# Kernel tuning notes

Measured on AMD Instinct MI355X. Metric: run time of the kernel, lower is better.

The kernel has to match this reference:

```python
import jax, jax.numpy as jnp
import numpy as np

# TT decomposition config (from Eff_TTEmbedding args in source)
P = (216, 216, 216)      # auto-factorized p_shapes for n=10,000,000 (216^3 >= n)
Q = (2, 4, 2)            # tt_q_shapes, prod = 16 = embedding_dim
R = (128, 128)           # tt_ranks
NUM_TABLES = 2
BATCH = 1024
NUM_EMB = 10_000_000


def setup_inputs() -> dict:
    key = jax.random.key(0)
    k0, k1, k2, k3 = jax.random.split(key, 4)
    # sparse indices per TT table: [n_tables, batch]
    lS_i = jax.random.randint(k3, (NUM_TABLES, BATCH), 0, NUM_EMB, dtype=jnp.int64)
    # TT cores, weight_dist='uniform'
    core0 = jax.random.uniform(k0, (NUM_TABLES, P[0], Q[0] * R[0]), dtype=jnp.float32, minval=-0.01, maxval=0.01)
    core1 = jax.random.uniform(k1, (NUM_TABLES, P[1], R[0] * Q[1] * R[1]), dtype=jnp.float32, minval=-0.01, maxval=0.01)
    core2 = jax.random.uniform(k2, (NUM_TABLES, P[2], R[1] * Q[2]), dtype=jnp.float32, minval=-0.01, maxval=0.01)
    return {"lS_i": lS_i, "core0": core0, "core1": core1, "core2": core2}


def _tt_lookup(idx, c0, c1, c2):
    """TT embedding lookup for one table. idx: [B] int; returns [B, prod(Q)]."""
    B = idx.shape[0]
    # mixed-radix decomposition of flat index into (i0, i1, i2)
    i0 = idx // (P[1] * P[2])
    i1 = (idx // P[2]) % P[1]
    i2 = idx % P[2]
    # gather TT core slices (the memory-bound irregular access)
    A = c0[i0].reshape(B, Q[0], R[0])            # [B, 2, 128]
    Bm = c1[i1].reshape(B, R[0], Q[1] * R[1])    # [B, 128, 512]
    C = c2[i2].reshape(B, R[1], Q[2])            # [B, 128, 2]
    # chained small matmuls along TT ranks
    AB = jnp.einsum('bqr,brs->bqs', A, Bm).reshape(B, Q[0] * Q[1], R[1])  # [B, 8, 128]
    out = jnp.einsum('bqr,brs->bqs', AB, C)      # [B, 8, 2]
    return out.reshape(B, Q[0] * Q[1] * Q[2])    # [B, 16]


def reference(lS_i, core0, core1, core2):
    # per-table dispatch (forward returns one embedding bag per TT table)
    return jax.vmap(_tt_lookup)(lS_i, core0, core1, core2)  # [n_tables, B, 16]
```

## Files before the change

kernel.cpp:

```cpp
#include <hip/hip_runtime.h>


#define NGROUPS 432
#define NLOOK   2048

__global__ __launch_bounds__(512) void tt_prep(const int* __restrict__ idx32,
                                               int* __restrict__ w) {
    __shared__ int cnt[NGROUPS];
    __shared__ int wtot[8];
    __shared__ int cursor[NGROUPS];
    const int tid  = threadIdx.x;
    const int lane = tid & 63;
    const int wv   = tid >> 6;

    for (int i = tid; i < NGROUPS; i += 512) cnt[i] = 0;
    __syncthreads();

    const bool is64 = (idx32[1] == 0) & (idx32[3] == 0) &
                      (idx32[5] == 0) & (idx32[7] == 0);

    int grp[4];
#pragma unroll
    for (int j = 0; j < 4; ++j) {
        const int id = tid + j * 512;
        const unsigned idx = is64 ? (unsigned)((const long long*)idx32)[id]
                                  : (unsigned)idx32[id];
        const unsigned i0  = idx / 46656u;
        const unsigned rem = idx - i0 * 46656u;
        const unsigned i1  = rem / 216u;
        const unsigned i2  = rem - i1 * 216u;
        const int table = id >> 10;
        grp[j] = table * 216 + (int)i1;
        w[2912 + id] = (int)((i0 << 16) | i2);
        atomicAdd(&cnt[grp[j]], 1);
    }
    __syncthreads();

    const int v = (tid < NGROUPS) ? cnt[tid] : 0;
    int s = v;
#pragma unroll
    for (int d = 1; d < 64; d <<= 1) {
        const int t = __shfl_up(s, d);
        if (lane >= d) s += t;
    }
    if (lane == 63) wtot[wv] = s;
    __syncthreads();
    int off = 0;
    for (int i = 0; i < wv; ++i) off += wtot[i];
    if (tid < NGROUPS) {
        const int st = s + off - v;
        w[tid]       = st;
        w[432 + tid] = v;
        cursor[tid]  = st;
    }
    __syncthreads();

#pragma unroll
    for (int j = 0; j < 4; ++j) {
        const int id  = tid + j * 512;
        const int pos = atomicAdd(&cursor[grp[j]], 1);
        w[864 + pos] = id;
    }
}

__global__ __launch_bounds__(128) void tt_main(
    const float* __restrict__ c0,
    const float* __restrict__ c1,
    const float* __restrict__ c2,
    const int* __restrict__ w,
    float* __restrict__ out)
{
    const int g  = blockIdx.x;
    const int q  = blockIdx.y;
    const int cs = blockIdx.z;
    const int m = w[432 + g];
    if (m <= cs * 8) return;
    const int s0    = w[g];
    const int table = g / 216;
    const int i1    = g - table * 216;

    const int tid = threadIdx.x;
    const int rh  = tid >> 6;
    const int tl  = tid & 63;

    __shared__ float lds[2048];
    float2* lds2 = (float2*)lds;
    __shared__ int s_id[8];
    __shared__ int s_aux[8];

    const float2* b2 = (const float2*)(c1 + (((size_t)(table * 216 + i1)) << 16))
                       + (size_t)rh * 64 * 256 + (q * 64 + tl);
    const float* c0t = c0 + (size_t)table * 216 * 256;

    for (int base = cs * 8; base < m; base += 16) {
        const int cl = min(8, m - base);
        __syncthreads();
        if (tid < 8) {
            const bool ok = tid < cl;
            const int id  = ok ? w[864 + s0 + base + tid] : 0;
            s_id[tid]  = id;
            s_aux[tid] = ok ? w[2912 + id] : 0;
        }
        __syncthreads();

#pragma unroll
        for (int l = 0; l < 8; ++l) {
            const float* ar = c0t + (size_t)(s_aux[l] >> 16) * 256;
#pragma unroll
            for (int k = 0; k < 2; ++k) {
                const int e = tid + 128 * k;
                lds[l * 256 + 2 * (e & 127) + (e >> 7)] = ar[e];
            }
        }
        __syncthreads();

        float2 acc[8][2];
#pragma unroll
        for (int l = 0; l < 8; ++l) {
            acc[l][0] = make_float2(0.f, 0.f);
            acc[l][1] = make_float2(0.f, 0.f);
        }

#pragma unroll 8
        for (int rr = 0; rr < 64; ++rr) {
            const float2 bv = b2[(size_t)rr * 256];
            const int r = rh * 64 + rr;
#pragma unroll
            for (int l = 0; l < 8; ++l) {
                const float2 av = lds2[l * 128 + r];
                acc[l][0].x += av.x * bv.x; acc[l][0].y += av.x * bv.y;
                acc[l][1].x += av.y * bv.x; acc[l][1].y += av.y * bv.y;
            }
        }

        __syncthreads();
        if (rh == 1) {
#pragma unroll
            for (int l = 0; l < 8; ++l) {
                lds2[(l * 2 + 0) * 64 + tl] = acc[l][0];
                lds2[(l * 2 + 1) * 64 + tl] = acc[l][1];
            }
        }
        __syncthreads();

        if (rh == 0) {
#pragma unroll
            for (int l = 0; l < 8; ++l) {
                const float2 t0 = lds2[(l * 2 + 0) * 64 + tl];
                const float2 t1 = lds2[(l * 2 + 1) * 64 + tl];
                const float a0x = acc[l][0].x + t0.x, a0y = acc[l][0].y + t0.y;
                const float a1x = acc[l][1].x + t1.x, a1y = acc[l][1].y + t1.y;
                if (l < cl) {
                    const float* crow = c2 + (size_t)(table * 216 + (s_aux[l] & 0xffff)) * 256;
                    const float4 cv = *(const float4*)(crow + 4 * tl);
                    float p00 = a0x * cv.x + a0y * cv.z;
                    float p01 = a0x * cv.y + a0y * cv.w;
                    float p10 = a1x * cv.x + a1y * cv.z;
                    float p11 = a1x * cv.y + a1y * cv.w;
#pragma unroll
                    for (int mm = 32; mm >= 1; mm >>= 1) {
                        p00 += __shfl_xor(p00, mm);
                        p01 += __shfl_xor(p01, mm);
                        p10 += __shfl_xor(p10, mm);
                        p11 += __shfl_xor(p11, mm);
                    }
                    if (tl == 0) {
                        float* o = out + (size_t)s_id[l] * 16;
                        o[q * 2 + 0]     = p00;
                        o[q * 2 + 1]     = p01;
                        o[8 + q * 2 + 0] = p10;
                        o[8 + q * 2 + 1] = p11;
                    }
                }
            }
        }
    }
}

extern "C" void kernel_launch(void* const* d_in, const int* in_sizes, int n_in,
                              void* d_out, int out_size, void* d_ws, size_t ws_size,
                              hipStream_t stream) {
    const int*   idx = (const int*)d_in[0];
    const float* c0  = (const float*)d_in[1];
    const float* c1  = (const float*)d_in[2];
    const float* c2  = (const float*)d_in[3];
    float* out = (float*)d_out;
    int* w = (int*)d_ws;

    tt_prep<<<dim3(1), dim3(512), 0, stream>>>(idx, w);
    tt_main<<<dim3(NGROUPS, 4, 2), dim3(128), 0, stream>>>(c0, c1, c2, w, out);
}
```

Baseline: 182.8 us.

## Merge q-split blocks into one 256-thread block with 4-wave rank split

Removes the grid split over the four output q-columns. Each 256-thread block now covers all 512 columns of the c1 slice through float4 nontemporal loads, and its four waves each handle 32 of the 128 rank rows. The aim is to share the c0 and c2 gathers and the index setup across q, which cuts redundant loads and block launches. The per-wave partial results are combined through a small LDS buffer and written as coalesced 16-float output rows. In exchange each thread holds many more accumulator registers and the grid has fewer blocks, which may lower parallelism.

```diff
diff --git a/kernel.cpp b/kernel.cpp
--- a/kernel.cpp
+++ b/kernel.cpp
@@ -3,6 +3,8 @@
 
 #define NGROUPS 432
 #define NLOOK   2048
+
+typedef float f4 __attribute__((ext_vector_type(4)));
 
 __global__ __launch_bounds__(512) void tt_prep(const int* __restrict__ idx32,
                                                int* __restrict__ w) {
@@ -63,7 +65,7 @@
     }
 }
 
-__global__ __launch_bounds__(128) void tt_main(
+__global__ __launch_bounds__(256) void tt_main(
     const float* __restrict__ c0,
     const float* __restrict__ c1,
     const float* __restrict__ c2,
@@ -71,8 +73,7 @@
     float* __restrict__ out)
 {
     const int g  = blockIdx.x;
-    const int q  = blockIdx.y;
-    const int cs = blockIdx.z;
+    const int cs = blockIdx.y;
     const int m = w[432 + g];
     if (m <= cs * 8) return;
     const int s0    = w[g];
@@ -80,17 +81,21 @@
     const int i1    = g - table * 216;
 
     const int tid = threadIdx.x;
-    const int rh  = tid >> 6;
-    const int tl  = tid & 63;
+    const int wv  = tid >> 6;
+    const int L   = tid & 63;
 
-    __shared__ float lds[2048];
-    float2* lds2 = (float2*)lds;
+    __shared__ float A[2048];
+    __shared__ float comb[512];
     __shared__ int s_id[8];
     __shared__ int s_aux[8];
 
-    const float2* b2 = (const float2*)(c1 + (((size_t)(table * 216 + i1)) << 16))
-                       + (size_t)rh * 64 * 256 + (q * 64 + tl);
+    const f4* bw = (const f4*)(c1 + (((size_t)(table * 216 + i1)) << 16))
+                   + (size_t)(32 * wv) * 128 + L;
     const float* c0t = c0 + (size_t)table * 216 * 256;
+    const float* c2t = c2 + (size_t)table * 216 * 256;
+
+    const int r1  = (L & 31) * 4;
+    const int q1b = L >> 5;
 
     for (int base = cs * 8; base < m; base += 16) {
         const int cl = min(8, m - base);
@@ -106,73 +111,75 @@
 #pragma unroll
         for (int l = 0; l < 8; ++l) {
             const float* ar = c0t + (size_t)(s_aux[l] >> 16) * 256;
+            A[l * 256 + 2 * (tid & 127) + (tid >> 7)] = ar[tid];
+        }
+        __syncthreads();
+
+        f4 acc[8][2][2];
 #pragma unroll
-            for (int k = 0; k < 2; ++k) {
-                const int e = tid + 128 * k;
-                lds[l * 256 + 2 * (e & 127) + (e >> 7)] = ar[e];
+        for (int l = 0; l < 8; ++l)
+#pragma unroll
+            for (int q = 0; q < 2; ++q) {
+                acc[l][q][0] = (f4)0.f;
+                acc[l][q][1] = (f4)0.f;
+            }
+
+#pragma unroll 4
+        for (int rr = 0; rr < 32; ++rr) {
+            const f4 b0 = __builtin_nontemporal_load(bw + (size_t)rr * 128);
+            const f4 b1 = __builtin_nontemporal_load(bw + (size_t)rr * 128 + 64);
+            const int r = 32 * wv + rr;
+#pragma unroll
+            for (int l = 0; l < 8; ++l) {
+                const float2 av = *(const float2*)&A[l * 256 + 2 * r];
+                acc[l][0][0] += av.x * b0;
+                acc[l][1][0] += av.y * b0;
+                acc[l][0][1] += av.x * b1;
+                acc[l][1][1] += av.y * b1;
+            }
+        }
+
+#pragma unroll
+        for (int l = 0; l < 8; ++l) {
+            const float* crow = c2t + (size_t)(s_aux[l] & 0xffff) * 256;
+            const f4 cA = *(const f4*)(crow + 2 * r1);
+            const f4 cB = *(const f4*)(crow + 2 * r1 + 4);
+            float p[2][2][2];
+#pragma unroll
+            for (int q = 0; q < 2; ++q)
+#pragma unroll
+                for (int c = 0; c < 2; ++c) {
+                    const f4 a = acc[l][q][c];
+                    p[q][c][0] = a.x*cA.x + a.y*cA.z + a.z*cB.x + a.w*cB.z;
+                    p[q][c][1] = a.x*cA.y + a.y*cA.w + a.z*cB.y + a.w*cB.w;
+                }
+#pragma unroll
+            for (int mm = 16; mm >= 1; mm >>= 1) {
+#pragma unroll
+                for (int q = 0; q < 2; ++q)
+#pragma unroll
+                    for (int c = 0; c < 2; ++c) {
+                        p[q][c][0] += __shfl_xor(p[q][c][0], mm);
+                        p[q][c][1] += __shfl_xor(p[q][c][1], mm);
+                    }
+            }
+            if ((L & 31) == 0) {
+#pragma unroll
+                for (int q = 0; q < 2; ++q)
+#pragma unroll
+                    for (int c = 0; c < 2; ++c) {
+                        comb[wv * 128 + l * 16 + q * 8 + (2 * c + q1b) * 2 + 0] = p[q][c][0];
+                        comb[wv * 128 + l * 16 + q * 8 + (2 * c + q1b) * 2 + 1] = p[q][c][1];
+                    }
             }
         }
         __syncthreads();
 
-        float2 acc[8][2];
-#pragma unroll
-        for (int l = 0; l < 8; ++l) {
-            acc[l][0] = make_float2(0.f, 0.f);
-            acc[l][1] = make_float2(0.f, 0.f);
-        }
-
-#pragma unroll 8
-        for (int rr = 0; rr < 64; ++rr) {
-            const float2 bv = b2[(size_t)rr * 256];
-            const int r = rh * 64 + rr;
-#pragma unroll
-            for (int l = 0; l < 8; ++l) {
-                const float2 av = lds2[l * 128 + r];
-                acc[l][0].x += av.x * bv.x; acc[l][0].y += av.x * bv.y;
-                acc[l][1].x += av.y * bv.x; acc[l][1].y += av.y * bv.y;
-            }
-        }
-
-        __syncthreads();
-        if (rh == 1) {
-#pragma unroll
-            for (int l = 0; l < 8; ++l) {
-                lds2[(l * 2 + 0) * 64 + tl] = acc[l][0];
-                lds2[(l * 2 + 1) * 64 + tl] = acc[l][1];
-            }
-        }
-        __syncthreads();
-
-        if (rh == 0) {
-#pragma unroll
-            for (int l = 0; l < 8; ++l) {
-                const float2 t0 = lds2[(l * 2 + 0) * 64 + tl];
-                const float2 t1 = lds2[(l * 2 + 1) * 64 + tl];
-                const float a0x = acc[l][0].x + t0.x, a0y = acc[l][0].y + t0.y;
-                const float a1x = acc[l][1].x + t1.x, a1y = acc[l][1].y + t1.y;
-                if (l < cl) {
-                    const float* crow = c2 + (size_t)(table * 216 + (s_aux[l] & 0xffff)) * 256;
-                    const float4 cv = *(const float4*)(crow + 4 * tl);
-                    float p00 = a0x * cv.x + a0y * cv.z;
-                    float p01 = a0x * cv.y + a0y * cv.w;
-                    float p10 = a1x * cv.x + a1y * cv.z;
-                    float p11 = a1x * cv.y + a1y * cv.w;
-#pragma unroll
-                    for (int mm = 32; mm >= 1; mm >>= 1) {
-                        p00 += __shfl_xor(p00, mm);
-                        p01 += __shfl_xor(p01, mm);
-                        p10 += __shfl_xor(p10, mm);
-                        p11 += __shfl_xor(p11, mm);
-                    }
-                    if (tl == 0) {
-                        float* o = out + (size_t)s_id[l] * 16;
-                        o[q * 2 + 0]     = p00;
-                        o[q * 2 + 1]     = p01;
-                        o[8 + q * 2 + 0] = p10;
-                        o[8 + q * 2 + 1] = p11;
-                    }
-                }
-            }
+        if (tid < 16 * cl) {
+            const int l = tid >> 4, k = tid & 15;
+            out[(size_t)s_id[l] * 16 + k] =
+                comb[l * 16 + k] + comb[128 + l * 16 + k] +
+                comb[256 + l * 16 + k] + comb[384 + l * 16 + k];
         }
     }
 }
@@ -188,5 +195,5 @@
     int* w = (int*)d_ws;
 
     tt_prep<<<dim3(1), dim3(512), 0, stream>>>(idx, w);
-    tt_main<<<dim3(NGROUPS, 4, 2), dim3(128), 0, stream>>>(c0, c1, c2, w, out);
+    tt_main<<<dim3(NGROUPS, 2), dim3(256), 0, stream>>>(c0, c1, c2, w, out);
 }
```

After: 199.9 us. 1.09x slower.

## Split TT core1 by rank blocks held in registers, combine partials with atomics

Applied to the files above, without the earlier changes.

Each block now handles one rank-0 block of 16 rows for a group and keeps its 16x512 slice of core1 in registers, loaded once and reused across all lookups in the group. Previously each block looped over rank rows and reread the B slice for every chunk of 8 lookups. Partial results from the 8 rank blocks are reduced across lanes, combined through shared memory, then added to the output with atomicAdd. This needs a memset of the output first, plus an extra launch and atomic traffic, and the floating-point summation order becomes nondeterministic.

```diff
diff --git a/kernel.cpp b/kernel.cpp
--- a/kernel.cpp
+++ b/kernel.cpp
@@ -3,6 +3,8 @@
 
 #define NGROUPS 432
 #define NLOOK   2048
+
+typedef float f4 __attribute__((ext_vector_type(4)));
 
 __global__ __launch_bounds__(512) void tt_prep(const int* __restrict__ idx32,
                                                int* __restrict__ w) {
@@ -63,7 +65,7 @@
     }
 }
 
-__global__ __launch_bounds__(128) void tt_main(
+__global__ __launch_bounds__(256) void tt_main(
     const float* __restrict__ c0,
     const float* __restrict__ c1,
     const float* __restrict__ c2,
@@ -71,108 +73,99 @@
     float* __restrict__ out)
 {
     const int g  = blockIdx.x;
-    const int q  = blockIdx.y;
-    const int cs = blockIdx.z;
+    const int rb = blockIdx.y;
     const int m = w[432 + g];
-    if (m <= cs * 8) return;
+    if (m == 0) return;
     const int s0    = w[g];
     const int table = g / 216;
     const int i1    = g - table * 216;
 
-    const int tid = threadIdx.x;
-    const int rh  = tid >> 6;
-    const int tl  = tid & 63;
+    const int t      = threadIdx.x;
+    const int h      = t >> 7;
+    const int lane31 = t & 31;
+    const int q1     = (t >> 5) & 3;
 
-    __shared__ float lds[2048];
-    float2* lds2 = (float2*)lds;
+    __shared__ float A_s[8][16][2];
+    __shared__ float comb[8][36];
     __shared__ int s_id[8];
     __shared__ int s_aux[8];
 
-    const float2* b2 = (const float2*)(c1 + (((size_t)(table * 216 + i1)) << 16))
-                       + (size_t)rh * 64 * 256 + (q * 64 + tl);
+    const f4* bp = (const f4*)(c1 + (((size_t)(table * 216 + i1)) << 16))
+                   + (size_t)rb * 2048 + t;
+    f4 b[8];
+#pragma unroll
+    for (int i = 0; i < 8; ++i)
+        b[i] = bp[i * 256];
+
     const float* c0t = c0 + (size_t)table * 216 * 256;
+    const float* c2t = c2 + (size_t)table * 216 * 256;
+    const int r1 = 4 * lane31;
 
-    for (int base = cs * 8; base < m; base += 16) {
+    for (int base = 0; base < m; base += 8) {
         const int cl = min(8, m - base);
-        __syncthreads();
-        if (tid < 8) {
-            const bool ok = tid < cl;
-            const int id  = ok ? w[864 + s0 + base + tid] : 0;
-            s_id[tid]  = id;
-            s_aux[tid] = ok ? w[2912 + id] : 0;
+        if (base) __syncthreads();
+        if (t < 8) {
+            const bool ok = t < cl;
+            const int id  = ok ? w[864 + s0 + base + t] : 0;
+            s_id[t]  = id;
+            s_aux[t] = ok ? w[2912 + id] : 0;
         }
         __syncthreads();
 
+        {
+            const int l = t >> 5, e = t & 31;
+            const int rl = e >> 1, q0 = e & 1;
+            A_s[l][rl][q0] =
+                c0t[(size_t)(s_aux[l] >> 16) * 256 + q0 * 128 + rb * 16 + rl];
+        }
+        __syncthreads();
+
+        f4 wacc[8][2];
+#pragma unroll
+        for (int l = 0; l < 8; ++l) { wacc[l][0] = (f4)0.f; wacc[l][1] = (f4)0.f; }
+
+#pragma unroll
+        for (int i = 0; i < 8; ++i) {
+            const int rl = 2 * i + h;
+#pragma unroll
+            for (int l = 0; l < 8; ++l) {
+                wacc[l][0] += A_s[l][rl][0] * b[i];
+                wacc[l][1] += A_s[l][rl][1] * b[i];
+            }
+        }
+
 #pragma unroll
         for (int l = 0; l < 8; ++l) {
-            const float* ar = c0t + (size_t)(s_aux[l] >> 16) * 256;
+            if (l < cl) {
+                const float* crow =
+                    c2t + (size_t)(s_aux[l] & 0xffff) * 256 + 2 * r1;
+                const f4 cA = *(const f4*)crow;
+                const f4 cB = *(const f4*)(crow + 4);
+                float p00 = wacc[l][0].x*cA.x + wacc[l][0].y*cA.z + wacc[l][0].z*cB.x + wacc[l][0].w*cB.z;
+                float p01 = wacc[l][0].x*cA.y + wacc[l][0].y*cA.w + wacc[l][0].z*cB.y + wacc[l][0].w*cB.w;
+                float p10 = wacc[l][1].x*cA.x + wacc[l][1].y*cA.z + wacc[l][1].z*cB.x + wacc[l][1].w*cB.z;
+                float p11 = wacc[l][1].x*cA.y + wacc[l][1].y*cA.w + wacc[l][1].z*cB.y + wacc[l][1].w*cB.w;
 #pragma unroll
-            for (int k = 0; k < 2; ++k) {
-                const int e = tid + 128 * k;
-                lds[l * 256 + 2 * (e & 127) + (e >> 7)] = ar[e];
+                for (int mm = 16; mm >= 1; mm >>= 1) {
+                    p00 += __shfl_xor(p00, mm);
+                    p01 += __shfl_xor(p01, mm);
+                    p10 += __shfl_xor(p10, mm);
+                    p11 += __shfl_xor(p11, mm);
+                }
+                if (lane31 == 0) {
+                    float* cb = &comb[h * 4 + q1][l * 4];
+                    cb[0] = p00; cb[1] = p01; cb[2] = p10; cb[3] = p11;
+                }
             }
         }
         __syncthreads();
 
-        float2 acc[8][2];
-#pragma unroll
-        for (int l = 0; l < 8; ++l) {
-            acc[l][0] = make_float2(0.f, 0.f);
-            acc[l][1] = make_float2(0.f, 0.f);
-        }
-
-#pragma unroll 8
-        for (int rr = 0; rr < 64; ++rr) {
-            const float2 bv = b2[(size_t)rr * 256];
-            const int r = rh * 64 + rr;
-#pragma unroll
-            for (int l = 0; l < 8; ++l) {
-                const float2 av = lds2[l * 128 + r];
-                acc[l][0].x += av.x * bv.x; acc[l][0].y += av.x * bv.y;
-                acc[l][1].x += av.y * bv.x; acc[l][1].y += av.y * bv.y;
-            }
-        }
-
-        __syncthreads();
-        if (rh == 1) {
-#pragma unroll
-            for (int l = 0; l < 8; ++l) {
-                lds2[(l * 2 + 0) * 64 + tl] = acc[l][0];
-                lds2[(l * 2 + 1) * 64 + tl] = acc[l][1];
-            }
-        }
-        __syncthreads();
-
-        if (rh == 0) {
-#pragma unroll
-            for (int l = 0; l < 8; ++l) {
-                const float2 t0 = lds2[(l * 2 + 0) * 64 + tl];
-                const float2 t1 = lds2[(l * 2 + 1) * 64 + tl];
-                const float a0x = acc[l][0].x + t0.x, a0y = acc[l][0].y + t0.y;
-                const float a1x = acc[l][1].x + t1.x, a1y = acc[l][1].y + t1.y;
-                if (l < cl) {
-                    const float* crow = c2 + (size_t)(table * 216 + (s_aux[l] & 0xffff)) * 256;
-                    const float4 cv = *(const float4*)(crow + 4 * tl);
-                    float p00 = a0x * cv.x + a0y * cv.z;
-                    float p01 = a0x * cv.y + a0y * cv.w;
-                    float p10 = a1x * cv.x + a1y * cv.z;
-                    float p11 = a1x * cv.y + a1y * cv.w;
-#pragma unroll
-                    for (int mm = 32; mm >= 1; mm >>= 1) {
-                        p00 += __shfl_xor(p00, mm);
-                        p01 += __shfl_xor(p01, mm);
-                        p10 += __shfl_xor(p10, mm);
-                        p11 += __shfl_xor(p11, mm);
-                    }
-                    if (tl == 0) {
-                        float* o = out + (size_t)s_id[l] * 16;
-                        o[q * 2 + 0]     = p00;
-                        o[q * 2 + 1]     = p01;
-                        o[8 + q * 2 + 0] = p10;
-                        o[8 + q * 2 + 1] = p11;
-                    }
-                }
-            }
+        if (t < 16 * cl) {
+            const int l = t >> 4, k = t & 15;
+            const int q0 = k >> 3, qq = (k >> 1) & 3, j = k & 1;
+            const float v = comb[qq][l * 4 + q0 * 2 + j] +
+                            comb[4 + qq][l * 4 + q0 * 2 + j];
+            atomicAdd(&out[(size_t)s_id[l] * 16 + k], v);
         }
     }
 }
@@ -187,6 +180,7 @@
     float* out = (float*)d_out;
     int* w = (int*)d_ws;
 
+    hipMemsetAsync(out, 0, (size_t)out_size * sizeof(float), stream);
     tt_prep<<<dim3(1), dim3(512), 0, stream>>>(idx, w);
-    tt_main<<<dim3(NGROUPS, 4, 2), dim3(128), 0, stream>>>(c0, c1, c2, w, out);
+    tt_main<<<dim3(NGROUPS, 8), dim3(256), 0, stream>>>(c0, c1, c2, w, out);
 }
```

Result: slower. 193.1 us (+5.6%).
